# Kernel optimization log

Measured on AMD Instinct MI355X. Metric: run time of the kernel, lower is better.

Reference implementation:

```python
import jax, jax.numpy as jnp
import numpy as np

N_NODES = 10000
HEADS = 4
NEG_SLOPE = 0.2


def gat_conv(x, src, dst, W, att_src, att_dst, bias, heads, ch):
    # x: [N, F_in]; W: [F_in, heads*ch]; att_*: [heads, ch]; bias: [heads*ch]
    N = x.shape[0]
    h = (x @ W).reshape(N, heads, ch)                       # [N, H, C]
    a_s = jnp.einsum('nhc,hc->nh', h, att_src)              # [N, H]
    a_d = jnp.einsum('nhc,hc->nh', h, att_dst)              # [N, H]
    e = jax.nn.leaky_relu(a_s[src] + a_d[dst], NEG_SLOPE)   # [E, H]
    # segment softmax over incoming edges of each dst node
    m = jax.ops.segment_max(e, dst, num_segments=N)         # [N, H]
    e = jnp.exp(e - m[dst])
    denom = jax.ops.segment_sum(e, dst, num_segments=N)     # [N, H]
    alpha = e / (denom[dst] + 1e-16)                        # [E, H]
    msg = h[src] * alpha[:, :, None]                        # [E, H, C]
    out = jax.ops.segment_sum(msg, dst, num_segments=N)     # [N, H, C]
    return out.reshape(N, heads * ch) + bias                # concat heads


def setup_inputs() -> dict:
    key = jax.random.key(0)
    ks = jax.random.split(key, 12)
    in_c, hid, out_c, H = 256, 64, 64, HEADS
    n_edges = 320000
    x = jax.random.normal(ks[0], (N_NODES, in_c), dtype=jnp.float32)
    edge_index = jax.random.randint(ks[1], (2, n_edges), 0, N_NODES, dtype=jnp.int64)

    def glorot(k, shape):
        fan = shape[0] + shape[-1]
        s = jnp.sqrt(6.0 / fan)
        return jax.random.uniform(k, shape, jnp.float32, -s, s)

    return {
        'x': x, 'edge_index': edge_index,
        'W1': glorot(ks[2], (in_c, H * hid)),
        'a1s': glorot(ks[3], (H, hid)), 'a1d': glorot(ks[4], (H, hid)),
        'b1': jnp.zeros((H * hid,), jnp.float32),
        'W2': glorot(ks[5], (H * hid, H * hid)),
        'a2s': glorot(ks[6], (H, hid)), 'a2d': glorot(ks[7], (H, hid)),
        'b2': jnp.zeros((H * hid,), jnp.float32),
        'W3': glorot(ks[8], (H * hid, H * out_c)),
        'a3s': glorot(ks[9], (H, out_c)), 'a3d': glorot(ks[10], (H, out_c)),
        'b3': jnp.zeros((H * out_c,), jnp.float32),
    }


def reference(x, edge_index, W1, a1s, a1d, b1, W2, a2s, a2d, b2, W3, a3s, a3d, b3):
    N = x.shape[0]
    # PyG GATConv default: add self loops
    loops = jnp.arange(N, dtype=edge_index.dtype)
    src = jnp.concatenate([edge_index[0], loops])
    dst = jnp.concatenate([edge_index[1], loops])
    hid, out_c = 64, 64
    h1 = jax.nn.elu(gat_conv(x, src, dst, W1, a1s, a1d, b1, HEADS, hid))
    h2 = jax.nn.elu(gat_conv(h1, src, dst, W2, a2s, a2d, b2, HEADS, hid))
    oup = jax.nn.elu(gat_conv(h2, src, dst, W3, a3s, a3d, b3, HEADS, out_c))
    return oup
```

## Files before the change

### kernel.cpp

```cpp
#include <hip/hip_runtime.h>
#include <hip/hip_bf16.h>

typedef __hip_bfloat16 bf16;
typedef __bf16 bf16x8v __attribute__((ext_vector_type(8)));
typedef float f32x4 __attribute__((ext_vector_type(4)));

#define CAP 128

__device__ __forceinline__ float bits2f(unsigned short u) {
  union { unsigned int i; float f; } c;
  c.i = ((unsigned int)u) << 16;
  return c.f;
}


__global__ void wt_zero_kernel(const float* __restrict__ W0, const float* __restrict__ W1,
                               const float* __restrict__ W2, bf16* __restrict__ Wt,
                               int* __restrict__ cnt, int N) {
  __shared__ float tile[16][17];
  int b = blockIdx.x;
  if (b < 768) {
    int L = b >> 8, rem = b & 255;
    const float* W = (L == 0) ? W0 : (L == 1) ? W1 : W2;
    bf16* T = Wt + (size_t)L * 65536;
    int n0 = (rem & 15) * 16, k0 = (rem >> 4) * 16;
    int tx = threadIdx.x & 15, ty = threadIdx.x >> 4;
    tile[ty][tx] = W[(k0 + ty) * 256 + n0 + tx];
    __syncthreads();
    T[(n0 + ty) * 256 + k0 + tx] = __float2bfloat16(tile[tx][ty]);
  } else {
    int idx = (b - 768) * 256 + threadIdx.x;
    if (idx < N) cnt[idx] = 0;
  }
}


template <bool FP32IN>
__device__ __forceinline__ void gemm_body(const void* __restrict__ Xv,
                                          const bf16* __restrict__ Wt,
                                          const float* __restrict__ att_s,
                                          const float* __restrict__ att_d,
                                          bf16* __restrict__ H, float* __restrict__ a_s,
                                          float* __restrict__ a_d, int M, int m0, int hd,
                                          bf16* As, bf16* Bs) {
  const int LDK = 136;
  int tid = threadIdx.x;
  int wave = tid >> 6, lane = tid & 63;
  int quad = lane >> 4, l16 = lane & 15;
  int n0 = hd * 64;
  int srow = tid >> 2;
  int koff = (tid & 3) * 32;

  const float* Xf = (const float*)Xv;
  const bf16*  Xb = (const bf16*)Xv;

  f32x4 acc[4] = {{0.f, 0.f, 0.f, 0.f}, {0.f, 0.f, 0.f, 0.f},
                  {0.f, 0.f, 0.f, 0.f}, {0.f, 0.f, 0.f, 0.f}};

  for (int ks = 0; ks < 256; ks += 128) {
    int gm = m0 + srow;
#pragma unroll
    for (int c = 0; c < 4; c++) {
      int ko = koff + c * 8;
      uint4 v;
      if (FP32IN) {
        float4 u0 = make_float4(0.f, 0.f, 0.f, 0.f), u1 = u0;
        if (gm < M) {
          u0 = *(const float4*)&Xf[gm * 256 + ks + ko];
          u1 = *(const float4*)&Xf[gm * 256 + ks + ko + 4];
        }
        union { bf16 h[8]; uint4 u; } pk;
        pk.h[0] = __float2bfloat16(u0.x); pk.h[1] = __float2bfloat16(u0.y);
        pk.h[2] = __float2bfloat16(u0.z); pk.h[3] = __float2bfloat16(u0.w);
        pk.h[4] = __float2bfloat16(u1.x); pk.h[5] = __float2bfloat16(u1.y);
        pk.h[6] = __float2bfloat16(u1.z); pk.h[7] = __float2bfloat16(u1.w);
        v = pk.u;
      } else {
        v = (gm < M) ? *(const uint4*)&Xb[gm * 256 + ks + ko]
                     : make_uint4(0u, 0u, 0u, 0u);
      }
      *(uint4*)&As[srow * LDK + ko] = v;
    }
#pragma unroll
    for (int c = 0; c < 4; c++) {
      int ko = koff + c * 8;
      *(uint4*)&Bs[srow * LDK + ko] = *(const uint4*)&Wt[(n0 + srow) * 256 + ks + ko];
    }
    __syncthreads();

#pragma unroll
    for (int kk = 0; kk < 4; kk++) {
      bf16x8v af = *(const bf16x8v*)&As[(wave * 16 + l16) * LDK + kk * 32 + quad * 8];
#pragma unroll
      for (int t = 0; t < 4; t++) {
        bf16x8v bfr = *(const bf16x8v*)&Bs[(t * 16 + l16) * LDK + kk * 32 + quad * 8];
        acc[t] = __builtin_amdgcn_mfma_f32_16x16x32_bf16(af, bfr, acc[t], 0, 0, 0);
      }
    }
    __syncthreads();
  }

  float ps[4] = {0.f, 0.f, 0.f, 0.f}, pd[4] = {0.f, 0.f, 0.f, 0.f};
#pragma unroll
  for (int t = 0; t < 4; t++) {
    float sa = att_s[hd * 64 + t * 16 + l16];
    float da = att_d[hd * 64 + t * 16 + l16];
#pragma unroll
    for (int j = 0; j < 4; j++) {
      int gm = m0 + wave * 16 + quad * 4 + j;
      float v = acc[t][j];
      if (gm < M) H[gm * 256 + n0 + t * 16 + l16] = __float2bfloat16(v);
      ps[j] += v * sa;
      pd[j] += v * da;
    }
  }
#pragma unroll
  for (int j = 0; j < 4; j++) {
#pragma unroll
    for (int s = 1; s < 16; s <<= 1) {
      ps[j] += __shfl_xor(ps[j], s, 64);
      pd[j] += __shfl_xor(pd[j], s, 64);
    }
    int gm = m0 + wave * 16 + quad * 4 + j;
    if (l16 == 0 && gm < M) {
      a_s[gm * 4 + hd] = ps[j];
      a_d[gm * 4 + hd] = pd[j];
    }
  }
}

__global__ void __launch_bounds__(256, 4)
gemm_mfma_kernel(const bf16* __restrict__ X, const bf16* __restrict__ Wt,
                 const float* __restrict__ att_s, const float* __restrict__ att_d,
                 bf16* __restrict__ H, float* __restrict__ a_s, float* __restrict__ a_d,
                 int M) {
  __shared__ bf16 As[64 * 136];
  __shared__ bf16 Bs[64 * 136];
  gemm_body<false>(X, Wt, att_s, att_d, H, a_s, a_d, M, blockIdx.x * 64, blockIdx.y,
                   As, Bs);
}

__global__ void __launch_bounds__(256, 4)
gemm1_fill_kernel(const float* __restrict__ X, const bf16* __restrict__ Wt,
                  const float* __restrict__ att_s, const float* __restrict__ att_d,
                  bf16* __restrict__ H, float* __restrict__ a_s, float* __restrict__ a_d,
                  int M, const int* __restrict__ ei, int E, int N,
                  int* __restrict__ cnt, int* __restrict__ csr, int ngb) {
  __shared__ bf16 As[64 * 136];
  __shared__ bf16 Bs[64 * 136];
  int b = blockIdx.x;
  if (b < ngb) {
    gemm_body<true>(X, Wt, att_s, att_d, H, a_s, a_d, M, (b >> 2) * 64, b & 3, As, Bs);
  } else {
    int t = (b - ngb) * 256 + threadIdx.x;
    if (t >= E + N) return;
    int src, dst;
    if (t < E) { src = ei[t]; dst = ei[E + t]; }
    else       { src = t - E; dst = t - E; }
    int pos = atomicAdd(&cnt[dst], 1);
    if (pos < CAP) csr[dst * CAP + pos] = src;
  }
}


__device__ __forceinline__ float4 ld_h(const bf16* __restrict__ H, int s, int ch4) {
  ushort4 u = *(const ushort4*)((const unsigned short*)H + (s << 8) + ch4);
  return make_float4(bits2f(u.x), bits2f(u.y), bits2f(u.z), bits2f(u.w));
}

template <bool FINAL>
__global__ void __launch_bounds__(256, 8)
agg_lds_kernel(const bf16* __restrict__ H, const float* __restrict__ a_s,
               const float* __restrict__ a_d, const int* __restrict__ cnt,
               const int* __restrict__ csr, const float* __restrict__ bias,
               bf16* __restrict__ OutB, float* __restrict__ OutF, int N) {
  __shared__ int   sIdx[CAP];
  __shared__ float sP[CAP * 4];
  __shared__ float sAcc[4][256];
  __shared__ float sS[4][64];
  int tid = threadIdx.x;
  int wave = tid >> 6, lane = tid & 63;
  int n = blockIdx.x;
  int head = lane >> 4;
  int ch4 = lane * 4;
  int deg = min(cnt[n], CAP);

  if (tid < deg) {
    int src = csr[n * CAP + tid];
    sIdx[tid] = src;
    float4 as4 = *(const float4*)&a_s[src * 4];
    float4 ad4 = *(const float4*)&a_d[n * 4];
    float4 e;
    e.x = as4.x + ad4.x; e.x = (e.x > 0.f) ? e.x : 0.2f * e.x;
    e.y = as4.y + ad4.y; e.y = (e.y > 0.f) ? e.y : 0.2f * e.y;
    e.z = as4.z + ad4.z; e.z = (e.z > 0.f) ? e.z : 0.2f * e.z;
    e.w = as4.w + ad4.w; e.w = (e.w > 0.f) ? e.w : 0.2f * e.w;
    float4 pv;
    pv.x = __expf(e.x); pv.y = __expf(e.y);
    pv.z = __expf(e.z); pv.w = __expf(e.w);
    *(float4*)&sP[tid * 4] = pv;
  }
  __syncthreads();

  int chunk = (deg + 3) >> 2;
  int j0 = wave * chunk;
  int j1 = min(j0 + chunk, deg);

  float s = 0.f;
  float4 acc = make_float4(0.f, 0.f, 0.f, 0.f);

  int j = j0;
  for (; j + 4 <= j1; j += 4) {
    int si[4]; float pw[4];
#pragma unroll
    for (int u = 0; u < 4; u++) { si[u] = sIdx[j + u]; pw[u] = sP[(j + u) * 4 + head]; }
    float4 h[4];
#pragma unroll
    for (int u = 0; u < 4; u++) h[u] = ld_h(H, si[u], ch4);
#pragma unroll
    for (int u = 0; u < 4; u++) {
      s += pw[u];
      acc.x += pw[u] * h[u].x;
      acc.y += pw[u] * h[u].y;
      acc.z += pw[u] * h[u].z;
      acc.w += pw[u] * h[u].w;
    }
  }
  for (; j < j1; j++) {
    int s0 = sIdx[j];
    float p0 = sP[j * 4 + head];
    float4 h0 = ld_h(H, s0, ch4);
    s += p0;
    acc.x += p0 * h0.x; acc.y += p0 * h0.y;
    acc.z += p0 * h0.z; acc.w += p0 * h0.w;
  }

  sS[wave][lane] = s;
  *(float4*)&sAcc[wave][ch4] = acc;
  __syncthreads();

  if (wave == 0) {
    float st = sS[0][lane] + sS[1][lane] + sS[2][lane] + sS[3][lane];
    float4 a0 = *(const float4*)&sAcc[0][ch4];
    float4 a1 = *(const float4*)&sAcc[1][ch4];
    float4 a2 = *(const float4*)&sAcc[2][ch4];
    float4 a3 = *(const float4*)&sAcc[3][ch4];
    float inv = 1.f / (st + 1e-16f);
    const float4 b4 = *(const float4*)&bias[ch4];
    float4 v;
    v.x = (a0.x + a1.x + a2.x + a3.x) * inv + b4.x;
    v.y = (a0.y + a1.y + a2.y + a3.y) * inv + b4.y;
    v.z = (a0.z + a1.z + a2.z + a3.z) * inv + b4.z;
    v.w = (a0.w + a1.w + a2.w + a3.w) * inv + b4.w;
    v.x = (v.x > 0.f) ? v.x : expm1f(v.x);
    v.y = (v.y > 0.f) ? v.y : expm1f(v.y);
    v.z = (v.z > 0.f) ? v.z : expm1f(v.z);
    v.w = (v.w > 0.f) ? v.w : expm1f(v.w);
    if (FINAL) {
      *(float4*)&OutF[n * 256 + ch4] = v;
    } else {
      union { bf16 h[4]; ushort4 u; } pk;
      pk.h[0] = __float2bfloat16(v.x); pk.h[1] = __float2bfloat16(v.y);
      pk.h[2] = __float2bfloat16(v.z); pk.h[3] = __float2bfloat16(v.w);
      *(ushort4*)((unsigned short*)OutB + n * 256 + ch4) = pk.u;
    }
  }
}


extern "C" void kernel_launch(void* const* d_in, const int* in_sizes, int n_in,
                              void* d_out, int out_size, void* d_ws, size_t ws_size,
                              hipStream_t stream) {
  const int N = in_sizes[0] / 256;
  const int E = in_sizes[1] / 2;

  const float* x  = (const float*)d_in[0];
  const int*   ei = (const int*)d_in[1];
  const float* Wl[3]  = {(const float*)d_in[2], (const float*)d_in[6], (const float*)d_in[10]};
  const float* asl[3] = {(const float*)d_in[3], (const float*)d_in[7], (const float*)d_in[11]};
  const float* adl[3] = {(const float*)d_in[4], (const float*)d_in[8], (const float*)d_in[12]};
  const float* bl[3]  = {(const float*)d_in[5], (const float*)d_in[9], (const float*)d_in[13]};
  float* out = (float*)d_out;

  char* p = (char*)d_ws;
  auto carve = [&](size_t bytes) {
    char* r = p;
    p += (bytes + 255) & ~size_t(255);
    return r;
  };
  int*   cnt     = (int*)carve(sizeof(int) * N);
  int*   csr     = (int*)carve(sizeof(int) * N * CAP);
  float* a_s     = (float*)carve(sizeof(float) * N * 4);
  float* a_d     = (float*)carve(sizeof(float) * N * 4);
  bf16*  Wt      = (bf16*)carve(sizeof(bf16) * 3 * 65536);
  bf16*  h_buf   = (bf16*)carve(sizeof(bf16) * N * 256);
  bf16*  x_buf   = (bf16*)carve(sizeof(bf16) * N * 256);
  (void)ws_size; (void)n_in; (void)out_size;

  const int zb = (N + 255) / 256;
  const int eb = (E + N + 255) / 256;
  const int ngb = ((N + 63) / 64) * 4;
  dim3 ggrid((N + 63) / 64, 4);

  wt_zero_kernel<<<768 + zb, 256, 0, stream>>>(Wl[0], Wl[1], Wl[2], Wt, cnt, N);
  gemm1_fill_kernel<<<ngb + eb, 256, 0, stream>>>(x, Wt, asl[0], adl[0], h_buf,
                                                  a_s, a_d, N, ei, E, N, cnt, csr, ngb);
  agg_lds_kernel<false><<<N, 256, 0, stream>>>(h_buf, a_s, a_d, cnt, csr, bl[0],
                                               x_buf, nullptr, N);
  gemm_mfma_kernel<<<ggrid, 256, 0, stream>>>(x_buf, Wt + 65536, asl[1], adl[1],
                                              h_buf, a_s, a_d, N);
  agg_lds_kernel<false><<<N, 256, 0, stream>>>(h_buf, a_s, a_d, cnt, csr, bl[1],
                                               x_buf, nullptr, N);
  gemm_mfma_kernel<<<ggrid, 256, 0, stream>>>(x_buf, Wt + 131072, asl[2], adl[2],
                                              h_buf, a_s, a_d, N);
  agg_lds_kernel<true><<<N, 256, 0, stream>>>(h_buf, a_s, a_d, cnt, csr, bl[2],
                                              nullptr, out, N);
}
```

Measured before the change: 200.7 us.

## Aggregate one destination node per wavefront with 16-byte feature loads

```diff
diff --git a/kernel.cpp b/kernel.cpp
--- a/kernel.cpp
+++ b/kernel.cpp
@@ -4,6 +4,7 @@
 typedef __hip_bfloat16 bf16;
 typedef __bf16 bf16x8v __attribute__((ext_vector_type(8)));
 typedef float f32x4 __attribute__((ext_vector_type(4)));
+typedef unsigned short u16x8 __attribute__((ext_vector_type(8)));
 
 #define CAP 128
 
@@ -163,106 +164,102 @@
 }
 
 
-__device__ __forceinline__ float4 ld_h(const bf16* __restrict__ H, int s, int ch4) {
-  ushort4 u = *(const ushort4*)((const unsigned short*)H + (s << 8) + ch4);
-  return make_float4(bits2f(u.x), bits2f(u.y), bits2f(u.z), bits2f(u.w));
-}
-
 template <bool FINAL>
 __global__ void __launch_bounds__(256, 8)
-agg_lds_kernel(const bf16* __restrict__ H, const float* __restrict__ a_s,
-               const float* __restrict__ a_d, const int* __restrict__ cnt,
-               const int* __restrict__ csr, const float* __restrict__ bias,
-               bf16* __restrict__ OutB, float* __restrict__ OutF, int N) {
-  __shared__ int   sIdx[CAP];
-  __shared__ float sP[CAP * 4];
-  __shared__ float sAcc[4][256];
-  __shared__ float sS[4][64];
+agg_wave_kernel(const bf16* __restrict__ H, const float* __restrict__ a_s,
+                const float* __restrict__ a_d, const int* __restrict__ cnt,
+                const int* __restrict__ csr, const float* __restrict__ bias,
+                bf16* __restrict__ OutB, float* __restrict__ OutF, int N) {
+  __shared__ int   wIdx[4][128];
+  __shared__ float wP[4][128 * 4];
   int tid = threadIdx.x;
   int wave = tid >> 6, lane = tid & 63;
-  int n = blockIdx.x;
-  int head = lane >> 4;
-  int ch4 = lane * 4;
-  int deg = min(cnt[n], CAP);
-
-  if (tid < deg) {
-    int src = csr[n * CAP + tid];
-    sIdx[tid] = src;
-    float4 as4 = *(const float4*)&a_s[src * 4];
+  int n = blockIdx.x * 4 + wave;
+
+  int deg = 0, degp = 0;
+  if (n < N) {
+    deg = min(cnt[n], CAP);
+    degp = (deg + 7) & ~7;
     float4 ad4 = *(const float4*)&a_d[n * 4];
-    float4 e;
-    e.x = as4.x + ad4.x; e.x = (e.x > 0.f) ? e.x : 0.2f * e.x;
-    e.y = as4.y + ad4.y; e.y = (e.y > 0.f) ? e.y : 0.2f * e.y;
-    e.z = as4.z + ad4.z; e.z = (e.z > 0.f) ? e.z : 0.2f * e.z;
-    e.w = as4.w + ad4.w; e.w = (e.w > 0.f) ? e.w : 0.2f * e.w;
-    float4 pv;
-    pv.x = __expf(e.x); pv.y = __expf(e.y);
-    pv.z = __expf(e.z); pv.w = __expf(e.w);
-    *(float4*)&sP[tid * 4] = pv;
+#pragma unroll
+    for (int base = 0; base < 2; base++) {
+      int jj = base * 64 + lane;
+      if (jj < deg) {
+        int src = csr[n * CAP + jj];
+        wIdx[wave][jj] = src;
+        float4 as4 = *(const float4*)&a_s[src * 4];
+        float4 e;
+        e.x = as4.x + ad4.x; e.x = (e.x > 0.f) ? e.x : 0.2f * e.x;
+        e.y = as4.y + ad4.y; e.y = (e.y > 0.f) ? e.y : 0.2f * e.y;
+        e.z = as4.z + ad4.z; e.z = (e.z > 0.f) ? e.z : 0.2f * e.z;
+        e.w = as4.w + ad4.w; e.w = (e.w > 0.f) ? e.w : 0.2f * e.w;
+        float4 pv;
+        pv.x = __expf(e.x); pv.y = __expf(e.y);
+        pv.z = __expf(e.z); pv.w = __expf(e.w);
+        *(float4*)&wP[wave][jj * 4] = pv;
+      }
+    }
+    int pad = degp - deg;
+    if (lane < pad) {
+      int jd = deg + lane;
+      wIdx[wave][jd] = 0;
+      *(float4*)&wP[wave][jd * 4] = make_float4(0.f, 0.f, 0.f, 0.f);
+    }
   }
   __syncthreads();
-
-  int chunk = (deg + 3) >> 2;
-  int j0 = wave * chunk;
-  int j1 = min(j0 + chunk, deg);
-
+  if (n >= N) return;
+
+  int sel = lane >> 5;
+  int l32 = lane & 31;
+  int c8 = l32 * 8;
+  int head = l32 >> 3;
+  const unsigned short* Hs = (const unsigned short*)H;
+
+  float acc[8] = {0.f, 0.f, 0.f, 0.f, 0.f, 0.f, 0.f, 0.f};
   float s = 0.f;
-  float4 acc = make_float4(0.f, 0.f, 0.f, 0.f);
-
-  int j = j0;
-  for (; j + 4 <= j1; j += 4) {
-    int si[4]; float pw[4];
-#pragma unroll
-    for (int u = 0; u < 4; u++) { si[u] = sIdx[j + u]; pw[u] = sP[(j + u) * 4 + head]; }
-    float4 h[4];
-#pragma unroll
-    for (int u = 0; u < 4; u++) h[u] = ld_h(H, si[u], ch4);
+  int npairp = degp >> 1;
+
+  for (int it = 0; it < npairp; it += 4) {
+    int   jv[4]; int sv[4]; float pv[4]; u16x8 hv[4];
+#pragma unroll
+    for (int u = 0; u < 4; u++) jv[u] = 2 * (it + u) + sel;
+#pragma unroll
+    for (int u = 0; u < 4; u++) sv[u] = wIdx[wave][jv[u]];
+#pragma unroll
+    for (int u = 0; u < 4; u++) pv[u] = wP[wave][jv[u] * 4 + head];
+#pragma unroll
+    for (int u = 0; u < 4; u++) hv[u] = *(const u16x8*)(Hs + sv[u] * 256 + c8);
 #pragma unroll
     for (int u = 0; u < 4; u++) {
-      s += pw[u];
-      acc.x += pw[u] * h[u].x;
-      acc.y += pw[u] * h[u].y;
-      acc.z += pw[u] * h[u].z;
-      acc.w += pw[u] * h[u].w;
-    }
-  }
-  for (; j < j1; j++) {
-    int s0 = sIdx[j];
-    float p0 = sP[j * 4 + head];
-    float4 h0 = ld_h(H, s0, ch4);
-    s += p0;
-    acc.x += p0 * h0.x; acc.y += p0 * h0.y;
-    acc.z += p0 * h0.z; acc.w += p0 * h0.w;
-  }
-
-  sS[wave][lane] = s;
-  *(float4*)&sAcc[wave][ch4] = acc;
-  __syncthreads();
-
-  if (wave == 0) {
-    float st = sS[0][lane] + sS[1][lane] + sS[2][lane] + sS[3][lane];
-    float4 a0 = *(const float4*)&sAcc[0][ch4];
-    float4 a1 = *(const float4*)&sAcc[1][ch4];
-    float4 a2 = *(const float4*)&sAcc[2][ch4];
-    float4 a3 = *(const float4*)&sAcc[3][ch4];
-    float inv = 1.f / (st + 1e-16f);
-    const float4 b4 = *(const float4*)&bias[ch4];
-    float4 v;
-    v.x = (a0.x + a1.x + a2.x + a3.x) * inv + b4.x;
-    v.y = (a0.y + a1.y + a2.y + a3.y) * inv + b4.y;
-    v.z = (a0.z + a1.z + a2.z + a3.z) * inv + b4.z;
-    v.w = (a0.w + a1.w + a2.w + a3.w) * inv + b4.w;
-    v.x = (v.x > 0.f) ? v.x : expm1f(v.x);
-    v.y = (v.y > 0.f) ? v.y : expm1f(v.y);
-    v.z = (v.z > 0.f) ? v.z : expm1f(v.z);
-    v.w = (v.w > 0.f) ? v.w : expm1f(v.w);
+      s += pv[u];
+#pragma unroll
+      for (int k = 0; k < 8; k++) acc[k] += pv[u] * bits2f(hv[u][k]);
+    }
+  }
+
+  s += __shfl_xor(s, 32, 64);
+#pragma unroll
+  for (int k = 0; k < 8; k++) acc[k] += __shfl_xor(acc[k], 32, 64);
+
+  if (sel == 0) {
+    float inv = 1.f / (s + 1e-16f);
+    float4 b0 = *(const float4*)&bias[c8];
+    float4 b1 = *(const float4*)&bias[c8 + 4];
+    float v[8];
+    v[0] = acc[0] * inv + b0.x; v[1] = acc[1] * inv + b0.y;
+    v[2] = acc[2] * inv + b0.z; v[3] = acc[3] * inv + b0.w;
+    v[4] = acc[4] * inv + b1.x; v[5] = acc[5] * inv + b1.y;
+    v[6] = acc[6] * inv + b1.z; v[7] = acc[7] * inv + b1.w;
+#pragma unroll
+    for (int k = 0; k < 8; k++) v[k] = (v[k] > 0.f) ? v[k] : expm1f(v[k]);
     if (FINAL) {
-      *(float4*)&OutF[n * 256 + ch4] = v;
+      *(float4*)&OutF[n * 256 + c8]     = make_float4(v[0], v[1], v[2], v[3]);
+      *(float4*)&OutF[n * 256 + c8 + 4] = make_float4(v[4], v[5], v[6], v[7]);
     } else {
-      union { bf16 h[4]; ushort4 u; } pk;
-      pk.h[0] = __float2bfloat16(v.x); pk.h[1] = __float2bfloat16(v.y);
-      pk.h[2] = __float2bfloat16(v.z); pk.h[3] = __float2bfloat16(v.w);
-      *(ushort4*)((unsigned short*)OutB + n * 256 + ch4) = pk.u;
+      union { bf16 h[8]; u16x8 u; } pk;
+#pragma unroll
+      for (int k = 0; k < 8; k++) pk.h[k] = __float2bfloat16(v[k]);
+      *(u16x8*)((unsigned short*)OutB + n * 256 + c8) = pk.u;
     }
   }
 }
@@ -300,19 +297,20 @@
   const int zb = (N + 255) / 256;
   const int eb = (E + N + 255) / 256;
   const int ngb = ((N + 63) / 64) * 4;
+  const int ab = (N + 3) / 4;
   dim3 ggrid((N + 63) / 64, 4);
 
   wt_zero_kernel<<<768 + zb, 256, 0, stream>>>(Wl[0], Wl[1], Wl[2], Wt, cnt, N);
   gemm1_fill_kernel<<<ngb + eb, 256, 0, stream>>>(x, Wt, asl[0], adl[0], h_buf,
                                                   a_s, a_d, N, ei, E, N, cnt, csr, ngb);
-  agg_lds_kernel<false><<<N, 256, 0, stream>>>(h_buf, a_s, a_d, cnt, csr, bl[0],
-                                               x_buf, nullptr, N);
+  agg_wave_kernel<false><<<ab, 256, 0, stream>>>(h_buf, a_s, a_d, cnt, csr, bl[0],
+                                                 x_buf, nullptr, N);
   gemm_mfma_kernel<<<ggrid, 256, 0, stream>>>(x_buf, Wt + 65536, asl[1], adl[1],
                                               h_buf, a_s, a_d, N);
-  agg_lds_kernel<false><<<N, 256, 0, stream>>>(h_buf, a_s, a_d, cnt, csr, bl[1],
-                                               x_buf, nullptr, N);
+  agg_wave_kernel<false><<<ab, 256, 0, stream>>>(h_buf, a_s, a_d, cnt, csr, bl[1],
+                                                 x_buf, nullptr, N);
   gemm_mfma_kernel<<<ggrid, 256, 0, stream>>>(x_buf, Wt + 131072, asl[2], adl[2],
                                               h_buf, a_s, a_d, N);
-  agg_lds_kernel<true><<<N, 256, 0, stream>>>(h_buf, a_s, a_d, cnt, csr, bl[2],
-                                              nullptr, out, N);
-}
+  agg_wave_kernel<true><<<ab, 256, 0, stream>>>(h_buf, a_s, a_d, cnt, csr, bl[2],
+                                                nullptr, out, N);
+}
```

Result: faster. 189.0 us (-5.8%).
